# Optimization experiments

Hardware: AMD Instinct MI355X
Metric: run time of the kernel (lower is better)

The kernel has to match this reference:

```python
import jax, jax.numpy as jnp
import numpy as np
from jax import lax

B, H, W_IN, C = 32, 32, 32, 128   # NHWC input
KH, KW = 3, 3                     # kernel size (padding 'same', stride 1)
F = 512                           # filters


def setup_inputs() -> dict:
    key = jax.random.key(0)
    ks = jax.random.split(key, 10)
    # sparse factor shapes: (KH*KW*C, 1152), (1152, F), (F, F)
    d0, d1, d2, d3 = KH * KW * C, 1152, F, F
    x = jax.random.normal(ks[0], (B, H, W_IN, C), dtype=jnp.float32)
    k0 = jax.random.normal(ks[1], (d0, d1), dtype=jnp.float32) * (1.0 / np.sqrt(d0))
    k1 = jax.random.normal(ks[2], (d1, d2), dtype=jnp.float32) * (1.0 / np.sqrt(d1))
    k2 = jax.random.normal(ks[3], (d2, d3), dtype=jnp.float32) * (1.0 / np.sqrt(d2))
    # fixed binary sparsity masks (K.constant in the original build)
    m0 = jax.random.bernoulli(ks[4], 0.1, (d0, d1)).astype(jnp.float32)
    m1 = jax.random.bernoulli(ks[5], 0.1, (d1, d2)).astype(jnp.float32)
    m2 = jax.random.bernoulli(ks[6], 0.1, (d2, d3)).astype(jnp.float32)
    scale = jax.random.normal(ks[7], (1,), dtype=jnp.float32)
    bias = jax.random.normal(ks[8], (F,), dtype=jnp.float32) * 0.01
    return {"x": x, "k0": k0, "k1": k1, "k2": k2,
            "m0": m0, "m1": m1, "m2": m2, "scale": scale, "bias": bias}


def reference(x, k0, k1, k2, m0, m1, m2, scale, bias):
    # Chained masked sparse factors collapse (associativity) to one effective
    # filter matrix of shape (KH*KW*C, F); the im2col row flatten order in the
    # original is (h, w, c), which matches an HWIO reshape exactly.
    w_eff = (k0 * m0) @ (k1 * m1) @ (k2 * m2)          # (KH*KW*C, F)
    w = (w_eff * scale[0]).reshape(KH, KW, C, F)        # fold scalar scale into kernel
    out = lax.conv_general_dilated(
        x, w, window_strides=(1, 1), padding='SAME',
        dimension_numbers=('NHWC', 'HWIO', 'NHWC'))     # (B, H, W, F)
    return out + bias
```

## Files before the change

kernel.cpp:

```cpp
#include <hip/hip_runtime.h>

typedef __attribute__((ext_vector_type(8))) short short8;
typedef __attribute__((ext_vector_type(4))) float f32x4;

typedef __attribute__((address_space(1))) const unsigned gas_u32;
typedef __attribute__((address_space(3))) unsigned las_u32;

static __device__ __forceinline__ void g2l16(const void* g, void* l) {
  __builtin_amdgcn_global_load_lds((gas_u32*)g, (las_u32*)l, 16, 0, 0);
}

static __device__ __forceinline__ short f2bf(float f) {
  union { float f; unsigned u; } v; v.f = f;
  unsigned r = (v.u + 0x7FFFu + ((v.u >> 16) & 1u)) >> 16;
  return (short)r;
}

#define MF(a_, b_, c_) __builtin_amdgcn_mfma_f32_16x16x32_bf16(a_, b_, c_, 0, 0, 0)

static __device__ __forceinline__ void xcvt_body(const float* __restrict__ x,
                                                 short* __restrict__ xbp, int i) {
  int c8 = i & 15;
  int t = i >> 4;
  int wp = t % 34, t2 = t / 34;
  int hp = t2 % 34, b = t2 / 34;
  short8 o = {};
  if (hp >= 1 && hp <= 32 && wp >= 1 && wp <= 32) {
    const f32x4* s = (const f32x4*)(x + (((size_t)((b << 5) + hp - 1) << 5) + (wp - 1)) * 128 + c8 * 8);
    f32x4 a = s[0], bb2 = s[1];
    o[0] = f2bf(a[0]); o[1] = f2bf(a[1]); o[2] = f2bf(a[2]); o[3] = f2bf(a[3]);
    o[4] = f2bf(bb2[0]); o[5] = f2bf(bb2[1]); o[6] = f2bf(bb2[2]); o[7] = f2bf(bb2[3]);
  }
  ((short8*)xbp)[i] = o;
}

__global__ __launch_bounds__(256) void k_prepw(const float* __restrict__ k0f,
                                               const float* __restrict__ m0f,
                                               const float* __restrict__ scf,
                                               const float* __restrict__ k1f,
                                               const float* __restrict__ m1f,
                                               const float* __restrict__ k2f,
                                               const float* __restrict__ m2f,
                                               short* __restrict__ w1b,
                                               short* __restrict__ w2T,
                                               short* __restrict__ w3T,
                                               const float* __restrict__ x,
                                               short* __restrict__ xbp) {
  __shared__ float tile[32][33];
  const int bb = blockIdx.x, tid = threadIdx.x;
  if (bb < 648) {
    int i = bb * 256 + tid;
    float s = scf[0];
    const f32x4* kk = (const f32x4*)k0f + (size_t)i * 2;
    const f32x4* mm = (const f32x4*)m0f + (size_t)i * 2;
    f32x4 a0 = kk[0], a1 = kk[1], b0 = mm[0], b1 = mm[1];
    short8 o;
    o[0] = f2bf(a0[0] * b0[0] * s); o[1] = f2bf(a0[1] * b0[1] * s);
    o[2] = f2bf(a0[2] * b0[2] * s); o[3] = f2bf(a0[3] * b0[3] * s);
    o[4] = f2bf(a1[0] * b1[0] * s); o[5] = f2bf(a1[1] * b1[1] * s);
    o[6] = f2bf(a1[2] * b1[2] * s); o[7] = f2bf(a1[3] * b1[3] * s);
    ((short8*)w1b)[i] = o;
  } else if (bb < 1480) {
    const float *kf, *mf; short* outp; int D, F, idx;
    if (bb < 1224) { kf = k1f; mf = m1f; outp = w2T; D = 1152; F = 512; idx = bb - 648; }
    else           { kf = k2f; mf = m2f; outp = w3T; D = 512;  F = 512; idx = bb - 1224; }
    int f0 = (idx & 15) * 32, d0 = (idx >> 4) * 32;
    int tx = tid & 31, ty = tid >> 5;
#pragma unroll
    for (int i = 0; i < 4; ++i) {
      int d = d0 + ty + i * 8;
      size_t ix = (size_t)d * F + f0 + tx;
      tile[ty + i * 8][tx] = kf[ix] * mf[ix];
    }
    __syncthreads();
#pragma unroll
    for (int i = 0; i < 4; ++i) {
      int f = f0 + ty + i * 8;
      outp[(size_t)f * D + d0 + tx] = f2bf(tile[tx][ty + i * 8]);
    }
  } else {
    xcvt_body(x, xbp, (bb - 1480) * 256 + tid);
  }
}

__global__ __launch_bounds__(256) void k_gemmx(const short* __restrict__ A,
                                               const short* __restrict__ BT,
                                               short* __restrict__ C, int M, int N, int K,
                                               const float* __restrict__ x,
                                               short* __restrict__ xbp, int xoff) {
  __shared__ __align__(16) short As[2][64][128];
  __shared__ __align__(16) short Bs[2][64][128];
  if (blockIdx.x >= 144) {
    xcvt_body(x, xbp, (xoff + (int)blockIdx.x - 144) * 256 + (int)threadIdx.x);
    return;
  }
  const int ntiles = N >> 6;
  const int m0 = (blockIdx.x / ntiles) << 6, n0 = (blockIdx.x % ntiles) << 6;
  const int tid = threadIdx.x;
  const int lane = tid & 63, wv = tid >> 6;
  const int wr = (wv >> 1) * 32, wc = (wv & 1) * 32;
  const int lr = lane & 15, lh = lane >> 4;

  const int rr = tid >> 4, sl = tid & 15;
  const int swz = sl ^ (rr & 7);
  const unsigned aOff = (unsigned)(m0 + rr) * K + swz * 8;
  const unsigned bOff = (unsigned)(n0 + rr) * K + swz * 8;
  const int ldsRow = 4 * wv;

  f32x4 acc[2][2] = {};

#define GST(buf_, kt_) do { \
    _Pragma("unroll") for (int j = 0; j < 4; ++j) \
      g2l16(A + aOff + (unsigned)j * 16u * (unsigned)K + (unsigned)(kt_) * 128u, \
            &As[buf_][j * 16 + ldsRow][0]); \
    _Pragma("unroll") for (int j = 0; j < 4; ++j) \
      g2l16(BT + bOff + (unsigned)j * 16u * (unsigned)K + (unsigned)(kt_) * 128u, \
            &Bs[buf_][j * 16 + ldsRow][0]); \
  } while (0)

  const int nk = K >> 7;
  GST(0, 0);
  asm volatile("s_waitcnt vmcnt(0)" ::: "memory");
  __builtin_amdgcn_s_barrier();

  for (int kt = 0; kt < nk; ++kt) {
    const int cur = kt & 1;
    if (kt + 1 < nk) { if (cur) GST(0, kt + 1); else GST(1, kt + 1); }
#pragma unroll
    for (int ks = 0; ks < 4; ++ks) {
      short8 af[2], bf[2];
#pragma unroll
      for (int i = 0; i < 2; ++i)
        af[i] = *(const short8*)&As[cur][wr + i * 16 + lr][((ks * 4 + lh) ^ (lr & 7)) * 8];
#pragma unroll
      for (int i = 0; i < 2; ++i)
        bf[i] = *(const short8*)&Bs[cur][wc + i * 16 + lr][((ks * 4 + lh) ^ (lr & 7)) * 8];
#pragma unroll
      for (int mi = 0; mi < 2; ++mi)
#pragma unroll
        for (int ni = 0; ni < 2; ++ni)
          acc[mi][ni] = MF(af[mi], bf[ni], acc[mi][ni]);
    }
    if (kt + 1 < nk) asm volatile("s_waitcnt vmcnt(0)" ::: "memory");
    __builtin_amdgcn_s_barrier();
  }
#pragma unroll
  for (int mi = 0; mi < 2; ++mi) {
    const int row = m0 + wr + mi * 16 + lh * 4;
#pragma unroll
    for (int ni = 0; ni < 2; ++ni) {
      const int col = n0 + wc + ni * 16 + lr;
#pragma unroll
      for (int q = 0; q < 4; ++q)
        C[(size_t)(row + q) * N + col] = f2bf(acc[mi][ni][q]);
    }
  }
#undef GST
}

#define RD_A(mf_, ks_) \
  (*(const short8*)&As[wr * 128 + (mf_) * 16 + lr][(((ks_) * 4 + lh) ^ (lr & 7)) * 8])
#define RD_B(nf_, ks_) \
  (*(const short8*)&Bs[wc * 64 + (nf_) * 16 + lr][(((ks_) * 4 + lh) ^ (lr & 7)) * 8])

#define LOADB do { \
  bfr[0][0] = RD_B(0, 0); bfr[0][1] = RD_B(0, 1); \
  bfr[1][0] = RD_B(1, 0); bfr[1][1] = RD_B(1, 1); \
  bfr[2][0] = RD_B(2, 0); bfr[2][1] = RD_B(2, 1); \
  bfr[3][0] = RD_B(3, 0); bfr[3][1] = RD_B(3, 1); } while (0)

#define STAGE_AQ(q_, tt_) do { \
  const int tc_ = (tt_) > 17 ? 17 : (tt_); \
  const int khw_ = tc_ >> 1; const int kh_ = (khw_ * 11) >> 5; const int kw_ = khw_ - kh_ * 3; \
  const int ao_ = (kh_ * 34 + kw_) * 128 + ((tc_ & 1) << 6) + (q_) * 4352; \
  g2l16(xbp + aBase + ao_, &As[(q_) * 32 + ldsA][0]); \
  g2l16(xbp + aBase + 17408 + ao_, &As[128 + (q_) * 32 + ldsA][0]); } while (0)

#define STAGE_B(tt_) do { \
  const int tc_ = (tt_) > 17 ? 17 : (tt_); \
  g2l16(wT + bBase +     tc_ * 64, &Bs[     ldsA][0]); \
  g2l16(wT + bBase + 36864 + tc_ * 64, &Bs[32 + ldsA][0]); \
  g2l16(wT + bBase + 73728 + tc_ * 64, &Bs[64 + ldsA][0]); \
  g2l16(wT + bBase + 110592 + tc_ * 64, &Bs[96 + ldsA][0]); } while (0)

#define MFMA16(p_) \
  acc[2*(p_)  ][0] = MF(a0k0, bfr[0][0], acc[2*(p_)  ][0]); \
  acc[2*(p_)  ][1] = MF(a0k0, bfr[1][0], acc[2*(p_)  ][1]); \
  acc[2*(p_)  ][2] = MF(a0k0, bfr[2][0], acc[2*(p_)  ][2]); \
  acc[2*(p_)  ][3] = MF(a0k0, bfr[3][0], acc[2*(p_)  ][3]); \
  acc[2*(p_)+1][0] = MF(a1k0, bfr[0][0], acc[2*(p_)+1][0]); \
  acc[2*(p_)+1][1] = MF(a1k0, bfr[1][0], acc[2*(p_)+1][1]); \
  acc[2*(p_)+1][2] = MF(a1k0, bfr[2][0], acc[2*(p_)+1][2]); \
  acc[2*(p_)+1][3] = MF(a1k0, bfr[3][0], acc[2*(p_)+1][3]); \
  acc[2*(p_)  ][0] = MF(a0k1, bfr[0][1], acc[2*(p_)  ][0]); \
  acc[2*(p_)  ][1] = MF(a0k1, bfr[1][1], acc[2*(p_)  ][1]); \
  acc[2*(p_)  ][2] = MF(a0k1, bfr[2][1], acc[2*(p_)  ][2]); \
  acc[2*(p_)  ][3] = MF(a0k1, bfr[3][1], acc[2*(p_)  ][3]); \
  acc[2*(p_)+1][0] = MF(a1k1, bfr[0][1], acc[2*(p_)+1][0]); \
  acc[2*(p_)+1][1] = MF(a1k1, bfr[1][1], acc[2*(p_)+1][1]); \
  acc[2*(p_)+1][2] = MF(a1k1, bfr[2][1], acc[2*(p_)+1][2]); \
  acc[2*(p_)+1][3] = MF(a1k1, bfr[3][1], acc[2*(p_)+1][3]);

#define PHASE(p_, PRE, WAITV, ...) do { \
  PRE; \
  short8 a0k0 = RD_A(2*(p_), 0),   a0k1 = RD_A(2*(p_), 1); \
  short8 a1k0 = RD_A(2*(p_)+1, 0), a1k1 = RD_A(2*(p_)+1, 1); \
  __VA_ARGS__ \
  asm volatile("s_waitcnt lgkmcnt(0)" ::: "memory"); \
  __builtin_amdgcn_sched_barrier(0); \
  __builtin_amdgcn_s_setprio(1); \
  MFMA16(p_) \
  __builtin_amdgcn_s_setprio(0); \
  WAITV; \
  __builtin_amdgcn_s_barrier(); \
} while (0)

#define VM4 asm volatile("s_waitcnt vmcnt(4)" ::: "memory")
#define VM6 asm volatile("s_waitcnt vmcnt(6)" ::: "memory")
#define VM8 asm volatile("s_waitcnt vmcnt(8)" ::: "memory")

__global__ __launch_bounds__(256, 2) void k_conv(const short* __restrict__ xbp,
                                                 const short* __restrict__ wT,
                                                 const float* __restrict__ bias,
                                                 float* __restrict__ out) {
  __shared__ __align__(16) short As[256][64];
  __shared__ __align__(16) short Bs[128][64];
  int bid = blockIdx.x;
  bid = (bid & 7) * 64 + (bid >> 3);
  const int mt = bid >> 2, nt = bid & 3;
  const int m0 = mt << 8, n0 = nt << 7;
  const int tid = threadIdx.x;
  const int lane = tid & 63, wid = tid >> 6;
  const int wr = wid >> 1, wc = wid & 1;
  const int lr = lane & 15, lh = lane >> 4;

  f32x4 acc[8][4] = {};
  short8 bfr[4][2];

  const int rsub = tid >> 3;
  const int sw = (tid & 7) ^ (rsub & 7);
  const int ldsA = wid * 8;

  const int Mb = m0 + rsub;
  const int b = Mb >> 10, h0 = (Mb >> 5) & 31, w = Mb & 31;
  const unsigned aBase = (unsigned)((b * 34 + h0) * 34 + w) * 128 + sw * 8;
  const unsigned bBase = (unsigned)(n0 + rsub) * 1152 + sw * 8;

  STAGE_B(0);
  STAGE_AQ(0, 0); STAGE_AQ(1, 0); STAGE_AQ(2, 0);
  asm volatile("s_waitcnt vmcnt(0)" ::: "memory");
  __builtin_amdgcn_s_barrier();

  for (int t = 0; t < 18; ++t) {
    const int tn = t + 1;
    PHASE(0, LOADB, VM4, STAGE_AQ(3, t););
    PHASE(1, ,      VM6, STAGE_B(tn););
    PHASE(2, ,      VM8, STAGE_AQ(0, tn); STAGE_AQ(1, tn););
    PHASE(3, ,      VM4, STAGE_AQ(2, tn););
  }
  asm volatile("s_waitcnt vmcnt(0)" ::: "memory");

  const int orow = m0 + wr * 128, ocol = n0 + wc * 64;
#pragma unroll
  for (int mf = 0; mf < 8; ++mf) {
    const int row = orow + mf * 16 + lh * 4;
#pragma unroll
    for (int nf = 0; nf < 4; ++nf) {
      const int col = ocol + nf * 16 + lr;
      const float bv = bias[col];
#pragma unroll
      for (int q = 0; q < 4; ++q)
        out[(size_t)(row + q) * 512 + col] = acc[mf][nf][q] + bv;
    }
  }
}

extern "C" void kernel_launch(void* const* d_in, const int* in_sizes, int n_in,
                              void* d_out, int out_size, void* d_ws, size_t ws_size,
                              hipStream_t stream) {
  (void)in_sizes; (void)n_in; (void)out_size; (void)ws_size;
  const float* x    = (const float*)d_in[0];
  const float* k0   = (const float*)d_in[1];
  const float* k1   = (const float*)d_in[2];
  const float* k2   = (const float*)d_in[3];
  const float* m0   = (const float*)d_in[4];
  const float* m1   = (const float*)d_in[5];
  const float* m2   = (const float*)d_in[6];
  const float* sc   = (const float*)d_in[7];
  const float* bias = (const float*)d_in[8];
  float* out = (float*)d_out;
  char* ws = (char*)d_ws;

  short* xbp = (short*)(ws);
  short* w1b = (short*)(ws + 9469952);
  short* w2T = (short*)(ws + 12124160);
  short* w3T = (short*)(ws + 13303808);
  short* A1b = (short*)(ws + 13828096);
  short* wET = (short*)(ws + 15007744);

  k_prepw<<<2248, 256, 0, stream>>>(k0, m0, sc, k1, m1, k2, m2, w1b, w2T, w3T, x, xbp);
  k_gemmx<<<916, 256, 0, stream>>>(w1b, w2T, A1b, 1152, 512, 1152, x, xbp, 768);
  k_gemmx<<<916, 256, 0, stream>>>(w3T, A1b, wET, 512, 1152, 512, x, xbp, 1540);
  k_conv<<<512, 256, 0, stream>>>(xbp, wET, bias, out);
}
```

Measured before the change: 69.28 us.

## Reassociate weight-chain GEMMs and overlap k0 mask conversion with first GEMM

```diff
diff --git a/kernel.cpp b/kernel.cpp
--- a/kernel.cpp
+++ b/kernel.cpp
@@ -17,6 +17,20 @@
 }
 
 #define MF(a_, b_, c_) __builtin_amdgcn_mfma_f32_16x16x32_bf16(a_, b_, c_, 0, 0, 0)
+
+static __device__ __forceinline__ void maskmul8(const float* __restrict__ k,
+                                                const float* __restrict__ m,
+                                                float s, short* __restrict__ o8, int i) {
+  const f32x4* kk = (const f32x4*)k + (size_t)i * 2;
+  const f32x4* mm = (const f32x4*)m + (size_t)i * 2;
+  f32x4 a0 = kk[0], a1 = kk[1], b0 = mm[0], b1 = mm[1];
+  short8 o;
+  o[0] = f2bf(a0[0] * b0[0] * s); o[1] = f2bf(a0[1] * b0[1] * s);
+  o[2] = f2bf(a0[2] * b0[2] * s); o[3] = f2bf(a0[3] * b0[3] * s);
+  o[4] = f2bf(a1[0] * b1[0] * s); o[5] = f2bf(a1[1] * b1[1] * s);
+  o[6] = f2bf(a1[2] * b1[2] * s); o[7] = f2bf(a1[3] * b1[3] * s);
+  ((short8*)o8)[i] = o;
+}
 
 static __device__ __forceinline__ void xcvt_body(const float* __restrict__ x,
                                                  short* __restrict__ xbp, int i) {
@@ -34,52 +48,36 @@
   ((short8*)xbp)[i] = o;
 }
 
-__global__ __launch_bounds__(256) void k_prepw(const float* __restrict__ k0f,
-                                               const float* __restrict__ m0f,
-                                               const float* __restrict__ scf,
-                                               const float* __restrict__ k1f,
+__global__ __launch_bounds__(256) void k_prep1(const float* __restrict__ k1f,
                                                const float* __restrict__ m1f,
                                                const float* __restrict__ k2f,
                                                const float* __restrict__ m2f,
-                                               short* __restrict__ w1b,
-                                               short* __restrict__ w2T,
+                                               short* __restrict__ w2b,
                                                short* __restrict__ w3T,
                                                const float* __restrict__ x,
                                                short* __restrict__ xbp) {
   __shared__ float tile[32][33];
   const int bb = blockIdx.x, tid = threadIdx.x;
-  if (bb < 648) {
-    int i = bb * 256 + tid;
-    float s = scf[0];
-    const f32x4* kk = (const f32x4*)k0f + (size_t)i * 2;
-    const f32x4* mm = (const f32x4*)m0f + (size_t)i * 2;
-    f32x4 a0 = kk[0], a1 = kk[1], b0 = mm[0], b1 = mm[1];
-    short8 o;
-    o[0] = f2bf(a0[0] * b0[0] * s); o[1] = f2bf(a0[1] * b0[1] * s);
-    o[2] = f2bf(a0[2] * b0[2] * s); o[3] = f2bf(a0[3] * b0[3] * s);
-    o[4] = f2bf(a1[0] * b1[0] * s); o[5] = f2bf(a1[1] * b1[1] * s);
-    o[6] = f2bf(a1[2] * b1[2] * s); o[7] = f2bf(a1[3] * b1[3] * s);
-    ((short8*)w1b)[i] = o;
-  } else if (bb < 1480) {
-    const float *kf, *mf; short* outp; int D, F, idx;
-    if (bb < 1224) { kf = k1f; mf = m1f; outp = w2T; D = 1152; F = 512; idx = bb - 648; }
-    else           { kf = k2f; mf = m2f; outp = w3T; D = 512;  F = 512; idx = bb - 1224; }
+  if (bb < 288) {
+    maskmul8(k1f, m1f, 1.0f, w2b, bb * 256 + tid);
+  } else if (bb < 544) {
+    const int idx = bb - 288;
     int f0 = (idx & 15) * 32, d0 = (idx >> 4) * 32;
     int tx = tid & 31, ty = tid >> 5;
 #pragma unroll
     for (int i = 0; i < 4; ++i) {
       int d = d0 + ty + i * 8;
-      size_t ix = (size_t)d * F + f0 + tx;
-      tile[ty + i * 8][tx] = kf[ix] * mf[ix];
+      size_t ix = (size_t)d * 512 + f0 + tx;
+      tile[ty + i * 8][tx] = k2f[ix] * m2f[ix];
     }
     __syncthreads();
 #pragma unroll
     for (int i = 0; i < 4; ++i) {
       int f = f0 + ty + i * 8;
-      outp[(size_t)f * D + d0 + tx] = f2bf(tile[tx][ty + i * 8]);
+      w3T[(size_t)f * 512 + d0 + tx] = f2bf(tile[tx][ty + i * 8]);
     }
   } else {
-    xcvt_body(x, xbp, (bb - 1480) * 256 + tid);
+    xcvt_body(x, xbp, (bb - 544) * 256 + tid);
   }
 }
 
@@ -87,11 +85,17 @@
                                                const short* __restrict__ BT,
                                                short* __restrict__ C, int M, int N, int K,
                                                const float* __restrict__ x,
-                                               short* __restrict__ xbp, int xoff) {
+                                               short* __restrict__ xbp, int xoff,
+                                               const float* __restrict__ mkf,
+                                               const float* __restrict__ mmf,
+                                               const float* __restrict__ mscf,
+                                               short* __restrict__ mout, int nmask) {
   __shared__ __align__(16) short As[2][64][128];
   __shared__ __align__(16) short Bs[2][64][128];
   if (blockIdx.x >= 144) {
-    xcvt_body(x, xbp, (xoff + (int)blockIdx.x - 144) * 256 + (int)threadIdx.x);
+    const int r = (int)blockIdx.x - 144;
+    if (r < nmask) maskmul8(mkf, mmf, mscf[0], mout, r * 256 + (int)threadIdx.x);
+    else xcvt_body(x, xbp, (xoff + r - nmask) * 256 + (int)threadIdx.x);
     return;
   }
   const int ntiles = N >> 6;
@@ -163,12 +167,6 @@
 #define RD_B(nf_, ks_) \
   (*(const short8*)&Bs[wc * 64 + (nf_) * 16 + lr][(((ks_) * 4 + lh) ^ (lr & 7)) * 8])
 
-#define LOADB do { \
-  bfr[0][0] = RD_B(0, 0); bfr[0][1] = RD_B(0, 1); \
-  bfr[1][0] = RD_B(1, 0); bfr[1][1] = RD_B(1, 1); \
-  bfr[2][0] = RD_B(2, 0); bfr[2][1] = RD_B(2, 1); \
-  bfr[3][0] = RD_B(3, 0); bfr[3][1] = RD_B(3, 1); } while (0)
-
 #define STAGE_AQ(q_, tt_) do { \
   const int tc_ = (tt_) > 17 ? 17 : (tt_); \
   const int khw_ = tc_ >> 1; const int kh_ = (khw_ * 11) >> 5; const int kw_ = khw_ - kh_ * 3; \
@@ -178,9 +176,9 @@
 
 #define STAGE_B(tt_) do { \
   const int tc_ = (tt_) > 17 ? 17 : (tt_); \
-  g2l16(wT + bBase +     tc_ * 64, &Bs[     ldsA][0]); \
-  g2l16(wT + bBase + 36864 + tc_ * 64, &Bs[32 + ldsA][0]); \
-  g2l16(wT + bBase + 73728 + tc_ * 64, &Bs[64 + ldsA][0]); \
+  g2l16(wT + bBase +          tc_ * 64, &Bs[     ldsA][0]); \
+  g2l16(wT + bBase +  36864 + tc_ * 64, &Bs[32 + ldsA][0]); \
+  g2l16(wT + bBase +  73728 + tc_ * 64, &Bs[64 + ldsA][0]); \
   g2l16(wT + bBase + 110592 + tc_ * 64, &Bs[96 + ldsA][0]); } while (0)
 
 #define MFMA16(p_) \
@@ -215,6 +213,12 @@
   __builtin_amdgcn_s_barrier(); \
 } while (0)
 
+#define LOADB do { \
+  bfr[0][0] = RD_B(0, 0); bfr[0][1] = RD_B(0, 1); \
+  bfr[1][0] = RD_B(1, 0); bfr[1][1] = RD_B(1, 1); \
+  bfr[2][0] = RD_B(2, 0); bfr[2][1] = RD_B(2, 1); \
+  bfr[3][0] = RD_B(3, 0); bfr[3][1] = RD_B(3, 1); } while (0)
+
 #define VM4 asm volatile("s_waitcnt vmcnt(4)" ::: "memory")
 #define VM6 asm volatile("s_waitcnt vmcnt(6)" ::: "memory")
 #define VM8 asm volatile("s_waitcnt vmcnt(8)" ::: "memory")
@@ -222,7 +226,7 @@
 __global__ __launch_bounds__(256, 2) void k_conv(const short* __restrict__ xbp,
                                                  const short* __restrict__ wT,
                                                  const float* __restrict__ bias,
-                                                 float* __restrict__ out) {
+                                                 float* __restrict__ outp) {
   __shared__ __align__(16) short As[256][64];
   __shared__ __align__(16) short Bs[128][64];
   int bid = blockIdx.x;
@@ -270,7 +274,7 @@
       const float bv = bias[col];
 #pragma unroll
       for (int q = 0; q < 4; ++q)
-        out[(size_t)(row + q) * 512 + col] = acc[mf][nf][q] + bv;
+        outp[(size_t)(row + q) * 512 + col] = acc[mf][nf][q] + bv;
     }
   }
 }
@@ -288,18 +292,22 @@
   const float* m2   = (const float*)d_in[6];
   const float* sc   = (const float*)d_in[7];
   const float* bias = (const float*)d_in[8];
-  float* out = (float*)d_out;
+  float* outp = (float*)d_out;
   char* ws = (char*)d_ws;
 
   short* xbp = (short*)(ws);
   short* w1b = (short*)(ws + 9469952);
-  short* w2T = (short*)(ws + 12124160);
+  short* w2b = (short*)(ws + 12124160);
   short* w3T = (short*)(ws + 13303808);
-  short* A1b = (short*)(ws + 13828096);
+  short* B1T = (short*)(ws + 13828096);
   short* wET = (short*)(ws + 15007744);
 
-  k_prepw<<<2248, 256, 0, stream>>>(k0, m0, sc, k1, m1, k2, m2, w1b, w2T, w3T, x, xbp);
-  k_gemmx<<<916, 256, 0, stream>>>(w1b, w2T, A1b, 1152, 512, 1152, x, xbp, 768);
-  k_gemmx<<<916, 256, 0, stream>>>(w3T, A1b, wET, 512, 1152, 512, x, xbp, 1540);
-  k_conv<<<512, 256, 0, stream>>>(xbp, wET, bias, out);
-}
+  k_prep1<<<1568, 256, 0, stream>>>(k1, m1, k2, m2, w2b, w3T, x, xbp);
+  k_gemmx<<<1304, 256, 0, stream>>>(w3T, w2b, B1T, 512, 1152, 512,
+                                    x, xbp, 1024, k0, m0, sc, w1b, 648);
+  k_gemmx<<<920, 256, 0, stream>>>(B1T, w1b, wET, 512, 1152, 1152,
+                                   x, xbp, 1536, (const float*)nullptr,
+                                   (const float*)nullptr, (const float*)nullptr,
+                                   (short*)nullptr, 0);
+  k_conv<<<512, 256, 0, stream>>>(xbp, wET, bias, outp);
+}
```

Result: no change. 69.22 us, median of 2 (-0.1%).
